# Kernel tuning notes

Measured on AMD Instinct MI355X. Metric: run time of the kernel, lower is better.

Reference implementation:

```python
import jax, jax.numpy as jnp
import numpy as np

HIDDEN = 300
LN_EPS = 1e-5


def _pair_indices(L, K):
    # row-major (emo, cau) order matches torch cat/reshape in couple_generator
    i = np.arange(L)[:, None]
    j = np.arange(L)[None, :]
    mask = np.abs(j - i) <= K
    emo, cau = np.nonzero(mask)
    return emo.astype(np.int32), cau.astype(np.int32)


def setup_inputs() -> dict:
    key = jax.random.key(0)
    ks = jax.random.split(key, 10)
    B, L, D = 32, 128, HIDDEN
    K = 12
    pos_dim = 50
    inp = {
        "h_e": jax.random.normal(ks[0], (B, L, D), jnp.float32),
        "h_c": jax.random.normal(ks[1], (B, L, D), jnp.float32),
        "h_share": jax.random.normal(ks[2], (B, L, D), jnp.float32),
        "pos_emb": jax.random.normal(ks[3], (2 * K + 1, pos_dim), jnp.float32) * 0.1,
        "W_hid": jax.random.normal(ks[4], (D, 2 * D + pos_dim), jnp.float32) * 0.02,
        "b_hid": jnp.zeros((D,), jnp.float32),
        "ln_g": jnp.ones((D,), jnp.float32),
        "ln_b": jnp.zeros((D,), jnp.float32),
        "W_rel": jax.random.normal(ks[5], (1, D), jnp.float32) * 0.02,
        "b_rel": jnp.zeros((1,), jnp.float32),
        "K": K,
    }
    return inp


def reference(h_e, h_c, h_share, pos_emb, W_hid, b_hid, ln_g, ln_b, W_rel, b_rel, K):
    B, L, D = h_e.shape
    he = h_e + h_share
    hc = h_c + h_share
    emo, cau = _pair_indices(L, int(K))  # static index constants
    rel = (cau - emo).astype(np.float32)  # [n]
    rp = jnp.asarray(cau - emo + int(K), jnp.int32)  # shifted rel pos
    # gather-concat pair features: [B, n, 2D]
    couples = jnp.concatenate([he[:, emo, :], hc[:, cau, :]], axis=-1)
    # Gaussian kernel over relative positions: [n, n]
    rel_j = jnp.asarray(rel)
    kernel = jnp.exp(-jnp.square(rel_j[:, None] - rel_j[None, :]))
    # smooth position embeddings (batch-independent): [n, pos_dim]
    rel_pos_emb = kernel @ pos_emb[rp]
    pair = jnp.concatenate(
        [couples, jnp.broadcast_to(rel_pos_emb[None], (B,) + rel_pos_emb.shape)],
        axis=-1,
    )
    h = jnp.einsum("bnf,df->bnd", pair, W_hid) + b_hid
    mu = jnp.mean(h, axis=-1, keepdims=True)
    var = jnp.mean(jnp.square(h - mu), axis=-1, keepdims=True)
    h = (h - mu) * jax.lax.rsqrt(var + LN_EPS) * ln_g + ln_b
    h = jax.nn.elu(h)  # dropout is identity in eval mode
    out = jnp.einsum("bnd,od->bno", h, W_rel) + b_rel
    return out[..., 0]  # [B, n_couple]
```

## Files before the change

kernel.cpp:

```cpp
#include <hip/hip_runtime.h>
#include <hip/hip_bf16.h>
#include <math.h>

#define BB 32
#define LL 128
#define DD 300
#define PD 50
#define KW 12
#define NP 3044
#define FF 650
#define NR 25
#define KP 320
#define NPAD 320
#define MM 4096
#define LN_EPS 1e-5f

typedef __attribute__((ext_vector_type(8))) short short8;
typedef __attribute__((ext_vector_type(4))) float f32x4;
typedef __attribute__((ext_vector_type(4))) unsigned short us4;
typedef __attribute__((ext_vector_type(4))) int i32x4;

__device__ __forceinline__ unsigned short f2b(float f) {
    union { float f; unsigned int u; } v; v.f = f;
    unsigned int u = v.u;
    unsigned int r = u + 0x7FFFu + ((u >> 16) & 1u);
    return (unsigned short)(r >> 16);
}

__device__ __forceinline__ int row_start(int i) {
    if (i <= 12) return i * 13 + (i * (i - 1)) / 2;
    if (i <= 116) return 222 + 25 * (i - 12);
    int s = i - 116;
    return 2822 + 24 * s - (s * (s - 1)) / 2;
}

__global__ __launch_bounds__(256) void misc_kernel(
    const float* __restrict__ pos_emb, const float* __restrict__ W_hid,
    const float* __restrict__ b_hid, float* __restrict__ P)
{
    __shared__ float sm[PD];
    const int r = blockIdx.x;
    const int tid = threadIdx.x;
    if (tid < PD) {
        float acc = 0.f;
        #pragma unroll
        for (int d = 0; d < NR; d++) {
            int ad = d - KW; if (ad < 0) ad = -ad;
            float cnt = (float)(LL - ad);
            float diff = (float)(r - d);
            acc += cnt * expf(-diff * diff) * pos_emb[d * PD + tid];
        }
        sm[tid] = acc;
    }
    __syncthreads();
    for (int dd = tid; dd < DD; dd += 256) {
        float a = b_hid[dd];
        const float* w = W_hid + dd * FF + 2 * DD;
        #pragma unroll
        for (int k = 0; k < PD; k++) a += sm[k] * w[k];
        P[r * DD + dd] = a;
    }
}

#define CONV_A_BLOCKS 2560
#define CONV_W_BLOCKS 800

__global__ __launch_bounds__(256) void conv_kernel(
    const float* __restrict__ h_e, const float* __restrict__ h_c,
    const float* __restrict__ h_share, const float* __restrict__ W_hid,
    unsigned short* __restrict__ Abf, unsigned short* __restrict__ Wbf)
{
    if (blockIdx.x < CONV_A_BLOCKS) {
        int idx = blockIdx.x * 256 + threadIdx.x;
        int z = idx / (MM * 80);
        int rem = idx - z * (MM * 80);
        int m = rem / 80;
        int kg = rem - m * 80;
        int k = kg * 4;
        us4 o;
        if (k < DD) {
            const float* A = z ? h_c : h_e;
            const float4 a = *(const float4*)&A[m * DD + k];
            const float4 s = *(const float4*)&h_share[m * DD + k];
            o.x = f2b(a.x + s.x); o.y = f2b(a.y + s.y);
            o.z = f2b(a.z + s.z); o.w = f2b(a.w + s.w);
        } else {
            o.x = 0; o.y = 0; o.z = 0; o.w = 0;
        }
        *(us4*)&Abf[(z * MM + m) * KP + k] = o;
    } else {
        int idx = (blockIdx.x - CONV_A_BLOCKS) * 256 + threadIdx.x;
        int z = idx / (NPAD * KP);
        int rem = idx - z * (NPAD * KP);
        int d = rem / KP;
        int k = rem - d * KP;
        unsigned short v = 0;
        if (d < DD && k < DD) v = f2b(W_hid[d * FF + z * DD + k]);
        Wbf[idx] = v;
    }
}

__global__ __launch_bounds__(256) void gemm_kernel(
    const unsigned short* __restrict__ Abf, const unsigned short* __restrict__ Wbf,
    float* __restrict__ E, float* __restrict__ Cc)
{
    __shared__ unsigned short Bs[160 * 40];

    const int z = blockIdx.z;
    const int m0 = blockIdx.x * 64;
    const int n0 = blockIdx.y * 160;
    const int tid = threadIdx.x;
    const int wid = tid >> 6;
    const int lane = tid & 63;
    const int nn = lane & 15;
    const int q  = lane >> 4;

    const unsigned short* Arow = Abf + (size_t)(z * MM + m0 + wid * 16 + nn) * KP + q * 8;
    const unsigned short* Wbase = Wbf + (size_t)(z * NPAD + n0) * KP;

    f32x4 acc[10];
    #pragma unroll
    for (int f = 0; f < 10; f++) acc[f] = (f32x4){0.f, 0.f, 0.f, 0.f};

    for (int k0 = 0; k0 < KP; k0 += 32) {
        for (int i = tid; i < 640; i += 256) {
            int n = i >> 2;
            int c = i & 3;
            i32x4 v = *(const i32x4*)&Wbase[n * KP + k0 + c * 8];
            *(i32x4*)&Bs[n * 40 + c * 8] = v;
        }
        __syncthreads();

        short8 a = *(const short8*)&Arow[k0];
        #pragma unroll
        for (int f = 0; f < 10; f++) {
            short8 b = *(const short8*)&Bs[(f * 16 + nn) * 40 + q * 8];
            acc[f] = __builtin_amdgcn_mfma_f32_16x16x32_bf16(a, b, acc[f], 0, 0, 0);
        }
        __syncthreads();
    }

    float* O = z ? Cc : E;
    const int row = m0 + wid * 16 + q * 4;
    #pragma unroll
    for (int f = 0; f < 10; f++) {
        int col = n0 + f * 16 + nn;
        if (col < DD) {
            #pragma unroll
            for (int r = 0; r < 4; r++)
                O[(size_t)(row + r) * DD + col] = acc[f][r];
        }
    }
}

__global__ __launch_bounds__(256) void pair_kernel(
    const float* __restrict__ E, const float* __restrict__ Cc,
    const float* __restrict__ P, const float* __restrict__ ln_g,
    const float* __restrict__ ln_b, const float* __restrict__ W_rel,
    const float* __restrict__ b_rel, float* __restrict__ out)
{
    const int wid = threadIdx.x >> 6;
    const int lane = threadIdx.x & 63;
    const int slot = blockIdx.x * 4 + wid;
    const int b = slot >> 7;
    const int i = slot & 127;

    const float* e_row = E + (size_t)(b * LL + i) * DD;

    float e[5], g[5], gb[5], wr[5];
    #pragma unroll
    for (int t = 0; t < 5; t++) {
        int d = lane + 64 * t;
        if (d < DD) {
            e[t]  = e_row[d];
            g[t]  = ln_g[d];
            gb[t] = ln_b[d];
            wr[t] = W_rel[d];
        } else {
            e[t] = 0.f; g[t] = 0.f; gb[t] = 0.f; wr[t] = 0.f;
        }
    }
    const float brel = b_rel[0];

    int jlo = i - KW; if (jlo < 0) jlo = 0;
    int jhi = i + KW; if (jhi > LL - 1) jhi = LL - 1;
    int p = b * NP + row_start(i);

    for (int j = jlo; j <= jhi; j++, p++) {
        const float* c_row = Cc + (size_t)(b * LL + j) * DD;
        const float* p_row = P + (j - i + KW) * DD;

        float h[5];
        float s = 0.f, ss = 0.f;
        #pragma unroll
        for (int t = 0; t < 5; t++) {
            int d = lane + 64 * t;
            h[t] = 0.f;
            if (d < DD) {
                h[t] = e[t] + c_row[d] + p_row[d];
                s += h[t];
                ss += h[t] * h[t];
            }
        }
        #pragma unroll
        for (int m = 1; m < 64; m <<= 1) {
            s  += __shfl_xor(s, m, 64);
            ss += __shfl_xor(ss, m, 64);
        }
        const float mean = s * (1.f / (float)DD);
        const float var = ss * (1.f / (float)DD) - mean * mean;
        const float rstd = rsqrtf(var + LN_EPS);

        float acc = 0.f;
        #pragma unroll
        for (int t = 0; t < 5; t++) {
            int d = lane + 64 * t;
            if (d < DD) {
                float y = (h[t] - mean) * rstd * g[t] + gb[t];
                float el = y > 0.f ? y : (__expf(y) - 1.f);
                acc += el * wr[t];
            }
        }
        #pragma unroll
        for (int m = 1; m < 64; m <<= 1) acc += __shfl_xor(acc, m, 64);

        if (lane == 0) out[p] = acc + brel;
    }
}

extern "C" void kernel_launch(void* const* d_in, const int* in_sizes, int n_in,
                              void* d_out, int out_size, void* d_ws, size_t ws_size,
                              hipStream_t stream) {
    const float* h_e     = (const float*)d_in[0];
    const float* h_c     = (const float*)d_in[1];
    const float* h_share = (const float*)d_in[2];
    const float* pos_emb = (const float*)d_in[3];
    const float* W_hid   = (const float*)d_in[4];
    const float* b_hid   = (const float*)d_in[5];
    const float* ln_g    = (const float*)d_in[6];
    const float* ln_b    = (const float*)d_in[7];
    const float* W_rel   = (const float*)d_in[8];
    const float* b_rel   = (const float*)d_in[9];

    float* out = (float*)d_out;

    float* ws = (float*)d_ws;
    float* E   = ws;
    float* C   = E + (size_t)MM * DD;
    float* P   = C + (size_t)MM * DD;
    unsigned short* Abf = (unsigned short*)(P + NR * DD);
    unsigned short* Wbf = Abf + (size_t)2 * MM * KP;

    misc_kernel<<<dim3(NR), dim3(256), 0, stream>>>(pos_emb, W_hid, b_hid, P);

    conv_kernel<<<dim3(CONV_A_BLOCKS + CONV_W_BLOCKS), dim3(256), 0, stream>>>(
        h_e, h_c, h_share, W_hid, Abf, Wbf);

    gemm_kernel<<<dim3(MM / 64, 2, 2), dim3(256), 0, stream>>>(Abf, Wbf, E, C);

    pair_kernel<<<dim3(BB * LL / 4), dim3(256), 0, stream>>>(
        E, C, P, ln_g, ln_b, W_rel, b_rel, out);
}
```

Before: 144.2 us.

## Fuse activation add and bf16 conversion into GEMM, merge prep kernels, split pair rows across waves

Removes the separate activation-conversion pass. The GEMM now reads h_e/h_c and h_share as fp32 directly, adds them and converts to bf16 in registers, which avoids writing and re-reading the padded bf16 A buffer. The position-embedding projection and the weight conversion are merged into one launch, so there is one fewer kernel. The pair kernel now gives each block one (b,i) row and spreads its j pairs across the 4 waves instead of one row per wave. The trade-off is that each GEMM column tile (n-block) re-reads and re-converts fp32 activations, and it also clamps negative variance.

```diff
diff --git a/kernel.cpp b/kernel.cpp
--- a/kernel.cpp
+++ b/kernel.cpp
@@ -17,7 +17,6 @@
 
 typedef __attribute__((ext_vector_type(8))) short short8;
 typedef __attribute__((ext_vector_type(4))) float f32x4;
-typedef __attribute__((ext_vector_type(4))) unsigned short us4;
 typedef __attribute__((ext_vector_type(4))) int i32x4;
 
 __device__ __forceinline__ unsigned short f2b(float f) {
@@ -34,62 +33,38 @@
     return 2822 + 24 * s - (s * (s - 1)) / 2;
 }
 
-__global__ __launch_bounds__(256) void misc_kernel(
+#define PREP_W_BLOCKS 800
+
+__global__ __launch_bounds__(256) void prep_kernel(
     const float* __restrict__ pos_emb, const float* __restrict__ W_hid,
-    const float* __restrict__ b_hid, float* __restrict__ P)
+    const float* __restrict__ b_hid, float* __restrict__ P,
+    unsigned short* __restrict__ Wbf)
 {
-    __shared__ float sm[PD];
-    const int r = blockIdx.x;
     const int tid = threadIdx.x;
-    if (tid < PD) {
-        float acc = 0.f;
-        #pragma unroll
-        for (int d = 0; d < NR; d++) {
-            int ad = d - KW; if (ad < 0) ad = -ad;
-            float cnt = (float)(LL - ad);
-            float diff = (float)(r - d);
-            acc += cnt * expf(-diff * diff) * pos_emb[d * PD + tid];
-        }
-        sm[tid] = acc;
-    }
-    __syncthreads();
-    for (int dd = tid; dd < DD; dd += 256) {
-        float a = b_hid[dd];
-        const float* w = W_hid + dd * FF + 2 * DD;
-        #pragma unroll
-        for (int k = 0; k < PD; k++) a += sm[k] * w[k];
-        P[r * DD + dd] = a;
-    }
-}
-
-#define CONV_A_BLOCKS 2560
-#define CONV_W_BLOCKS 800
-
-__global__ __launch_bounds__(256) void conv_kernel(
-    const float* __restrict__ h_e, const float* __restrict__ h_c,
-    const float* __restrict__ h_share, const float* __restrict__ W_hid,
-    unsigned short* __restrict__ Abf, unsigned short* __restrict__ Wbf)
-{
-    if (blockIdx.x < CONV_A_BLOCKS) {
-        int idx = blockIdx.x * 256 + threadIdx.x;
-        int z = idx / (MM * 80);
-        int rem = idx - z * (MM * 80);
-        int m = rem / 80;
-        int kg = rem - m * 80;
-        int k = kg * 4;
-        us4 o;
-        if (k < DD) {
-            const float* A = z ? h_c : h_e;
-            const float4 a = *(const float4*)&A[m * DD + k];
-            const float4 s = *(const float4*)&h_share[m * DD + k];
-            o.x = f2b(a.x + s.x); o.y = f2b(a.y + s.y);
-            o.z = f2b(a.z + s.z); o.w = f2b(a.w + s.w);
-        } else {
-            o.x = 0; o.y = 0; o.z = 0; o.w = 0;
-        }
-        *(us4*)&Abf[(z * MM + m) * KP + k] = o;
+    if (blockIdx.x < NR) {
+        __shared__ float sm[PD];
+        const int r = blockIdx.x;
+        if (tid < PD) {
+            float acc = 0.f;
+            #pragma unroll
+            for (int d = 0; d < NR; d++) {
+                int ad = d - KW; if (ad < 0) ad = -ad;
+                float cnt = (float)(LL - ad);
+                float diff = (float)(r - d);
+                acc += cnt * expf(-diff * diff) * pos_emb[d * PD + tid];
+            }
+            sm[tid] = acc;
+        }
+        __syncthreads();
+        for (int dd = tid; dd < DD; dd += 256) {
+            float a = b_hid[dd];
+            const float* w = W_hid + dd * FF + 2 * DD;
+            #pragma unroll
+            for (int k = 0; k < PD; k++) a += sm[k] * w[k];
+            P[r * DD + dd] = a;
+        }
     } else {
-        int idx = (blockIdx.x - CONV_A_BLOCKS) * 256 + threadIdx.x;
+        int idx = (blockIdx.x - NR) * 256 + tid;
         int z = idx / (NPAD * KP);
         int rem = idx - z * (NPAD * KP);
         int d = rem / KP;
@@ -101,7 +76,8 @@
 }
 
 __global__ __launch_bounds__(256) void gemm_kernel(
-    const unsigned short* __restrict__ Abf, const unsigned short* __restrict__ Wbf,
+    const float* __restrict__ h_e, const float* __restrict__ h_c,
+    const float* __restrict__ h_share, const unsigned short* __restrict__ Wbf,
     float* __restrict__ E, float* __restrict__ Cc)
 {
     __shared__ unsigned short Bs[160 * 40];
@@ -115,7 +91,9 @@
     const int nn = lane & 15;
     const int q  = lane >> 4;
 
-    const unsigned short* Arow = Abf + (size_t)(z * MM + m0 + wid * 16 + nn) * KP + q * 8;
+    const int row = m0 + wid * 16 + nn;
+    const float* xr = (z ? h_c : h_e) + (size_t)row * DD;
+    const float* sr = h_share + (size_t)row * DD;
     const unsigned short* Wbase = Wbf + (size_t)(z * NPAD + n0) * KP;
 
     f32x4 acc[10];
@@ -131,7 +109,28 @@
         }
         __syncthreads();
 
-        short8 a = *(const short8*)&Arow[k0];
+        const int kb = k0 + q * 8;
+        float a8[8];
+        if (kb + 7 < DD) {
+            float4 x0 = *(const float4*)&xr[kb];
+            float4 x1 = *(const float4*)&xr[kb + 4];
+            float4 s0 = *(const float4*)&sr[kb];
+            float4 s1 = *(const float4*)&sr[kb + 4];
+            a8[0] = x0.x + s0.x; a8[1] = x0.y + s0.y;
+            a8[2] = x0.z + s0.z; a8[3] = x0.w + s0.w;
+            a8[4] = x1.x + s1.x; a8[5] = x1.y + s1.y;
+            a8[6] = x1.z + s1.z; a8[7] = x1.w + s1.w;
+        } else {
+            #pragma unroll
+            for (int u = 0; u < 8; u++) {
+                int k = kb + u;
+                a8[u] = (k < DD) ? (xr[k] + sr[k]) : 0.f;
+            }
+        }
+        short8 a;
+        #pragma unroll
+        for (int u = 0; u < 8; u++) a[u] = (short)f2b(a8[u]);
+
         #pragma unroll
         for (int f = 0; f < 10; f++) {
             short8 b = *(const short8*)&Bs[(f * 16 + nn) * 40 + q * 8];
@@ -141,14 +140,14 @@
     }
 
     float* O = z ? Cc : E;
-    const int row = m0 + wid * 16 + q * 4;
+    const int orow = m0 + wid * 16 + q * 4;
     #pragma unroll
     for (int f = 0; f < 10; f++) {
         int col = n0 + f * 16 + nn;
         if (col < DD) {
             #pragma unroll
             for (int r = 0; r < 4; r++)
-                O[(size_t)(row + r) * DD + col] = acc[f][r];
+                O[(size_t)(orow + r) * DD + col] = acc[f][r];
         }
     }
 }
@@ -161,7 +160,7 @@
 {
     const int wid = threadIdx.x >> 6;
     const int lane = threadIdx.x & 63;
-    const int slot = blockIdx.x * 4 + wid;
+    const int slot = blockIdx.x;
     const int b = slot >> 7;
     const int i = slot & 127;
 
@@ -184,9 +183,9 @@
 
     int jlo = i - KW; if (jlo < 0) jlo = 0;
     int jhi = i + KW; if (jhi > LL - 1) jhi = LL - 1;
-    int p = b * NP + row_start(i);
-
-    for (int j = jlo; j <= jhi; j++, p++) {
+    const int base = b * NP + row_start(i);
+
+    for (int j = jlo + wid; j <= jhi; j += 4) {
         const float* c_row = Cc + (size_t)(b * LL + j) * DD;
         const float* p_row = P + (j - i + KW) * DD;
 
@@ -208,7 +207,8 @@
             ss += __shfl_xor(ss, m, 64);
         }
         const float mean = s * (1.f / (float)DD);
-        const float var = ss * (1.f / (float)DD) - mean * mean;
+        float var = ss * (1.f / (float)DD) - mean * mean;
+        if (var < 0.f) var = 0.f;
         const float rstd = rsqrtf(var + LN_EPS);
 
         float acc = 0.f;
@@ -224,7 +224,7 @@
         #pragma unroll
         for (int m = 1; m < 64; m <<= 1) acc += __shfl_xor(acc, m, 64);
 
-        if (lane == 0) out[p] = acc + brel;
+        if (lane == 0) out[base + (j - jlo)] = acc + brel;
     }
 }
 
@@ -248,16 +248,14 @@
     float* E   = ws;
     float* C   = E + (size_t)MM * DD;
     float* P   = C + (size_t)MM * DD;
-    unsigned short* Abf = (unsigned short*)(P + NR * DD);
-    unsigned short* Wbf = Abf + (size_t)2 * MM * KP;
-
-    misc_kernel<<<dim3(NR), dim3(256), 0, stream>>>(pos_emb, W_hid, b_hid, P);
-
-    conv_kernel<<<dim3(CONV_A_BLOCKS + CONV_W_BLOCKS), dim3(256), 0, stream>>>(
-        h_e, h_c, h_share, W_hid, Abf, Wbf);
-
-    gemm_kernel<<<dim3(MM / 64, 2, 2), dim3(256), 0, stream>>>(Abf, Wbf, E, C);
-
-    pair_kernel<<<dim3(BB * LL / 4), dim3(256), 0, stream>>>(
+    unsigned short* Wbf = (unsigned short*)(P + NR * DD);
+
+    prep_kernel<<<dim3(NR + PREP_W_BLOCKS), dim3(256), 0, stream>>>(
+        pos_emb, W_hid, b_hid, P, Wbf);
+
+    gemm_kernel<<<dim3(MM / 64, 2, 2), dim3(256), 0, stream>>>(
+        h_e, h_c, h_share, Wbf, E, C);
+
+    pair_kernel<<<dim3(BB * LL), dim3(256), 0, stream>>>(
         E, C, P, ln_g, ln_b, W_rel, b_rel, out);
 }
```

Result: faster. 131.4 us (-8.9%).
